# Kernel optimization log

Measured on AMD Instinct MI355X. Metric: run time of the kernel, lower is better.

## Reference

```python
import jax, jax.numpy as jnp
import numpy as np

N_U = 100000   # user nodes
N_V = 100000   # item nodes
D = 64         # input_dim
O = 64         # output_dim
R = 5          # num_support (rating levels)
E = 500000     # edges per relation


def setup_inputs() -> dict:
    key = jax.random.key(0)
    ks = jax.random.split(key, 8)
    init_range = np.sqrt(6.0 / (D + O))
    return {
        "x_u": jax.random.normal(ks[0], (N_U, D), jnp.float32),
        "x_v": jax.random.normal(ks[1], (N_V, D), jnp.float32),
        "weights_u": jax.random.uniform(ks[2], (R, D, O), jnp.float32, -init_range, init_range),
        "weights_v": jax.random.uniform(ks[3], (R, D, O), jnp.float32, -init_range, init_range),
        "bias_u": jnp.full((O,), 0.01, jnp.float32),
        "bias_v": jnp.full((O,), 0.01, jnp.float32),
        "edge_val": jax.random.uniform(ks[4], (R, E), jnp.float32),
        "edge_u": jax.random.randint(ks[5], (R, E), 0, N_U, jnp.int32),
        "edge_v": jax.random.randint(ks[6], (R, E), 0, N_V, jnp.int32),
    }


def reference(x_u, x_v, weights_u, weights_v, bias_u, bias_v, edge_val, edge_u, edge_v):
    # Cumulative (ordinal mixture) weights: wu_i = sum_{j<=i} W_u[j]
    Wu = jnp.cumsum(weights_u, axis=0)          # [R, D, O]
    Wv = jnp.cumsum(weights_v, axis=0)          # [R, D, O]

    tmp_u = jnp.einsum("nd,rdo->rno", x_u, Wu)  # [R, N_U, O]
    tmp_v = jnp.einsum("md,rdo->rmo", x_v, Wv)  # [R, N_V, O]

    gather = jax.vmap(lambda t, idx: t[idx])    # per-relation row gather

    # z_u = sum_r support_r @ tmp_v_r : scatter edge messages into user rows
    msg_u = (edge_val[..., None] * gather(tmp_v, edge_v)).reshape(R * E, O)
    z_u = jax.ops.segment_sum(msg_u, edge_u.reshape(-1), num_segments=N_U)

    # z_v = sum_r support_r^T @ tmp_u_r : scatter into item rows
    msg_v = (edge_val[..., None] * gather(tmp_u, edge_u)).reshape(R * E, O)
    z_v = jax.ops.segment_sum(msg_v, edge_v.reshape(-1), num_segments=N_V)

    u_out = jax.nn.relu(z_u + bias_u)
    v_out = jax.nn.relu(z_v + bias_v)
    return (u_out, v_out)
```

## Files before the change

kernel.cpp:

```cpp
#include <hip/hip_runtime.h>

#define N_U 100000
#define N_V 100000
#define OO 64
#define RR 5
#define EE 500000
#define TOT_E (RR * EE)
#define NB 782
#define CAP 4096
#define CAPU 3584
#define SCAT_BLOCKS 306
#define GEMM_BLOCKS 391

typedef short bf16x8 __attribute__((ext_vector_type(8)));
typedef float f32x4 __attribute__((ext_vector_type(4)));

__device__ __forceinline__ float bf2f(unsigned short u) {
  union { unsigned int i; float f; } x;
  x.i = ((unsigned int)u) << 16;
  return x.f;
}
__device__ __forceinline__ unsigned short f2bf(float f) {
  union { float f; unsigned int i; } x;
  x.f = f;
  unsigned int lsb = (x.i >> 16) & 1u;
  unsigned int r = x.i + 0x7fffu + lsb;
  return (unsigned short)(r >> 16);
}

__global__ void prep_weights(const float* __restrict__ wu,
                             const float* __restrict__ wv,
                             unsigned short* __restrict__ bfrag,
                             unsigned* __restrict__ gcur) {
  int side = blockIdx.x;
  if (gcur) {
    unsigned* g = gcur + side * 1024;
    for (int i = threadIdx.x; i < NB; i += 256) g[i] = (unsigned)i * CAP;
  }
  const float* w = side ? wv : wu;
  for (int idx = threadIdx.x; idx < 4096; idx += 256) {
    int d = idx >> 6, o = idx & 63;
    int c = o >> 4, n = o & 15;
    int sk = d >> 5, q = (d >> 3) & 3, jj = d & 7;
    int f = c * 2 + sk;
    int lane = q * 16 + n;
    int pos = (f * 64 + lane) * 8 + jj;
    float acc = 0.f;
    for (int r = 0; r < RR; ++r) {
      acc += w[r * 4096 + idx];
      bfrag[(side * RR + r) * 4096 + pos] = f2bf(acc);
    }
  }
}

__global__ __launch_bounds__(1024) void mega(
    const int* __restrict__ dst0, const int* __restrict__ src0,
    const int* __restrict__ dst1, const int* __restrict__ src1,
    const float* __restrict__ val,
    unsigned* __restrict__ gcur0, unsigned* __restrict__ keyP0,
    unsigned short* __restrict__ valP0,
    unsigned* __restrict__ gcur1, unsigned* __restrict__ keyP1,
    unsigned short* __restrict__ valP1,
    const float* __restrict__ X,
    const unsigned short* __restrict__ bfrag_side,
    unsigned short* __restrict__ tmp5,
    int nS0, int nS1) {
  __shared__ unsigned lds_u32[18972];
  int blk = blockIdx.x;
  int tid = threadIdx.x;
  if (blk < nS0 + nS1) {
    bool sB = (blk >= nS0);
    const int* dst = sB ? dst1 : dst0;
    const int* src = sB ? src1 : src0;
    unsigned* gcursor = sB ? gcur1 : gcur0;
    unsigned* keyP = sB ? keyP1 : keyP0;
    unsigned short* valP = sB ? valP1 : valP0;
    int sblk = sB ? blk - nS0 : blk;

    unsigned* skey = lds_u32;
    unsigned short* sval = (unsigned short*)(lds_u32 + 8192);
    unsigned short* sbid = (unsigned short*)(lds_u32 + 12288);
    unsigned* cnt  = lds_u32 + 16384;
    unsigned* sc   = lds_u32 + 17166;
    unsigned* gbase = lds_u32 + 18190;
    for (int i = tid; i < NB; i += 1024) cnt[i] = 0u;
    __syncthreads();
    int base = sblk * 8192;
    int t8 = base + tid * 8;
    bool full = (t8 < TOT_E);
    if (full) {
      int4 d0 = *(const int4*)(dst + t8);
      int4 d1 = *(const int4*)(dst + t8 + 4);
      atomicAdd(&cnt[d0.x >> 7], 1u);
      atomicAdd(&cnt[d0.y >> 7], 1u);
      atomicAdd(&cnt[d0.z >> 7], 1u);
      atomicAdd(&cnt[d0.w >> 7], 1u);
      atomicAdd(&cnt[d1.x >> 7], 1u);
      atomicAdd(&cnt[d1.y >> 7], 1u);
      atomicAdd(&cnt[d1.z >> 7], 1u);
      atomicAdd(&cnt[d1.w >> 7], 1u);
    }
    __syncthreads();
    sc[tid] = (tid < NB) ? cnt[tid] : 0u;
    __syncthreads();
    for (int off = 1; off < 1024; off <<= 1) {
      unsigned a = sc[tid];
      unsigned b = (tid >= off) ? sc[tid - off] : 0u;
      __syncthreads();
      sc[tid] = a + b;
      __syncthreads();
    }
    for (int b = tid; b < NB; b += 1024) {
      unsigned c = cnt[b];
      gbase[b] = c ? atomicAdd(&gcursor[b], c) : 0u;
      cnt[b] = sc[b] - c;
    }
    __syncthreads();
    unsigned total = sc[NB - 1];
    __syncthreads();
    for (int b = tid; b < NB; b += 1024) sc[b] = cnt[b];
    __syncthreads();
    if (full) {
      int4 d0 = *(const int4*)(dst + t8);
      int4 d1 = *(const int4*)(dst + t8 + 4);
      int4 s0 = *(const int4*)(src + t8);
      int4 s1 = *(const int4*)(src + t8 + 4);
      float4 v0 = *(const float4*)(val + t8);
      float4 v1 = *(const float4*)(val + t8 + 4);
      unsigned rb = (unsigned)(t8 / EE) * N_U;
#define PUT(dd, ss, vv)                                                     \
      {                                                                     \
        int bb = (dd) >> 7;                                                 \
        unsigned pos = atomicAdd(&sc[bb], 1u);                              \
        skey[pos] = (((unsigned)((dd) & 127)) << 19) | (rb + (unsigned)(ss)); \
        sval[pos] = f2bf(vv);                                               \
        sbid[pos] = (unsigned short)bb;                                     \
      }
      PUT(d0.x, s0.x, v0.x)
      PUT(d0.y, s0.y, v0.y)
      PUT(d0.z, s0.z, v0.z)
      PUT(d0.w, s0.w, v0.w)
      PUT(d1.x, s1.x, v1.x)
      PUT(d1.y, s1.y, v1.y)
      PUT(d1.z, s1.z, v1.z)
      PUT(d1.w, s1.w, v1.w)
#undef PUT
    }
    __syncthreads();
    for (int i = tid; i < (int)total; i += 1024) {
      unsigned b = sbid[i];
      unsigned addr = gbase[b] + ((unsigned)i - cnt[b]);
      keyP[addr] = skey[i];
      valP[addr] = sval[i];
    }
  } else {
    unsigned short* smem = (unsigned short*)lds_u32;
    for (int i = tid; i < 2560; i += 1024)
      ((bf16x8*)smem)[i] = ((const bf16x8*)bfrag_side)[i];
    __syncthreads();
    int lane = tid & 63;
    int wave = tid >> 6;
    int q = lane >> 4, m = lane & 15;
    int t = (blk - nS0 - nS1) * 16 + wave;
    if (t >= N_U / 16) return;
    int r0 = t * 16;
    const float* xr = X + (size_t)(r0 + m) * 64;
    float4 p0 = *(const float4*)(xr + q * 8);
    float4 p1 = *(const float4*)(xr + q * 8 + 4);
    float4 p2 = *(const float4*)(xr + 32 + q * 8);
    float4 p3 = *(const float4*)(xr + 32 + q * 8 + 4);
    bf16x8 a0, a1;
    a0[0] = (short)f2bf(p0.x); a0[1] = (short)f2bf(p0.y);
    a0[2] = (short)f2bf(p0.z); a0[3] = (short)f2bf(p0.w);
    a0[4] = (short)f2bf(p1.x); a0[5] = (short)f2bf(p1.y);
    a0[6] = (short)f2bf(p1.z); a0[7] = (short)f2bf(p1.w);
    a1[0] = (short)f2bf(p2.x); a1[1] = (short)f2bf(p2.y);
    a1[2] = (short)f2bf(p2.z); a1[3] = (short)f2bf(p2.w);
    a1[4] = (short)f2bf(p3.x); a1[5] = (short)f2bf(p3.y);
    a1[6] = (short)f2bf(p3.z); a1[7] = (short)f2bf(p3.w);
    for (int r = 0; r < RR; ++r) {
      f32x4 acc[4];
#pragma unroll
      for (int c = 0; c < 4; ++c) {
        bf16x8 b0 = *(const bf16x8*)(smem + r * 4096 + ((c * 2 + 0) * 64 + lane) * 8);
        bf16x8 b1 = *(const bf16x8*)(smem + r * 4096 + ((c * 2 + 1) * 64 + lane) * 8);
        f32x4 a = {0.f, 0.f, 0.f, 0.f};
        a = __builtin_amdgcn_mfma_f32_16x16x32_bf16(a0, b0, a, 0, 0, 0);
        a = __builtin_amdgcn_mfma_f32_16x16x32_bf16(a1, b1, a, 0, 0, 0);
        acc[c] = a;
      }
      unsigned short* trow = tmp5 + (size_t)r * N_U * 64;
#pragma unroll
      for (int i = 0; i < 4; ++i) {
        ushort4 o;
        o.x = f2bf(acc[0][i]); o.y = f2bf(acc[1][i]);
        o.z = f2bf(acc[2][i]); o.w = f2bf(acc[3][i]);
        *(ushort4*)(trow + (size_t)(r0 + q * 4 + i) * 64 + m * 4) = o;
      }
    }
  }
}

__global__ __launch_bounds__(512, 8) void bucket_sort_agg(
    const unsigned* __restrict__ keyP, const unsigned short* __restrict__ valP,
    const unsigned* __restrict__ gcursor,
    const unsigned short* __restrict__ tmp5,
    const float* __restrict__ bias, float* __restrict__ out) {
  __shared__ unsigned okey[CAP];
  __shared__ unsigned short oval[CAP];
  __shared__ unsigned hist[128];
  __shared__ unsigned starts[129];
  __shared__ unsigned cur[128];
  int b = blockIdx.x;
  unsigned base = (unsigned)b * CAP;
  int cnt = (int)(gcursor[b] - base);
  if (cnt > CAPU) cnt = CAPU;
  for (int i = threadIdx.x; i < 128; i += 512) hist[i] = 0u;
  __syncthreads();
  for (int i = threadIdx.x; i < cnt; i += 512)
    atomicAdd(&hist[keyP[base + i] >> 19], 1u);
  __syncthreads();
  if (threadIdx.x == 0) {
    unsigned acc = 0u;
    for (int l = 0; l < 128; ++l) {
      starts[l] = acc;
      acc += (hist[l] + 3u) & ~3u;
    }
    starts[128] = acc;
  }
  __syncthreads();
  unsigned tot = starts[128];
  for (int i = threadIdx.x; i < (int)tot; i += 512) { okey[i] = 0u; oval[i] = 0; }
  for (int l = threadIdx.x; l < 128; l += 512) cur[l] = starts[l];
  __syncthreads();
  for (int i = threadIdx.x; i < cnt; i += 512) {
    unsigned k = keyP[base + i];
    unsigned pos = atomicAdd(&cur[k >> 19], 1u);
    okey[pos] = k & 0x7FFFFu;
    oval[pos] = valP[base + i];
  }
  __syncthreads();

  int lane = threadIdx.x & 63;
  int wave = threadIdx.x >> 6;
  int g16 = lane >> 4;
  int m = lane & 15;
  int nb0 = b * 128;
  int nodes = (N_U - nb0 < 128) ? (N_U - nb0) : 128;
  const unsigned short* tp = tmp5 + (m << 2);
  float bl = bias[lane];
  for (int l = wave; l < nodes; l += 8) {
    unsigned s = starts[l];
    unsigned e = starts[l + 1];
    float a0 = 0.f, a1 = 0.f, a2 = 0.f, a3 = 0.f;
    unsigned k = s;
    for (; k + 8 <= e; k += 8) {
      unsigned key0 = okey[k + g16];
      unsigned key1 = okey[k + 4 + g16];
      float v0 = bf2f(oval[k + g16]);
      float v1 = bf2f(oval[k + 4 + g16]);
      ushort4 t0 = *(const ushort4*)(tp + (size_t)key0 * 64);
      ushort4 t1 = *(const ushort4*)(tp + (size_t)key1 * 64);
      a0 += v0 * bf2f(t0.x);
      a1 += v0 * bf2f(t0.y);
      a2 += v0 * bf2f(t0.z);
      a3 += v0 * bf2f(t0.w);
      a0 += v1 * bf2f(t1.x);
      a1 += v1 * bf2f(t1.y);
      a2 += v1 * bf2f(t1.z);
      a3 += v1 * bf2f(t1.w);
    }
    if (k < e) {
      unsigned key0 = okey[k + g16];
      float v0 = bf2f(oval[k + g16]);
      ushort4 t0 = *(const ushort4*)(tp + (size_t)key0 * 64);
      a0 += v0 * bf2f(t0.x);
      a1 += v0 * bf2f(t0.y);
      a2 += v0 * bf2f(t0.z);
      a3 += v0 * bf2f(t0.w);
    }
    a0 += __shfl_xor(a0, 16); a0 += __shfl_xor(a0, 32);
    a1 += __shfl_xor(a1, 16); a1 += __shfl_xor(a1, 32);
    a2 += __shfl_xor(a2, 16); a2 += __shfl_xor(a2, 32);
    a3 += __shfl_xor(a3, 16); a3 += __shfl_xor(a3, 32);
    float r = (g16 & 2) ? ((g16 & 1) ? a3 : a2) : ((g16 & 1) ? a1 : a0);
    out[(size_t)(nb0 + l) * 64 + lane] = fmaxf(r + bl, 0.f);
  }
}

__global__ __launch_bounds__(256) void gemm_kernel(
    const float* __restrict__ X, const unsigned short* __restrict__ bfrag,
    unsigned short* __restrict__ tmp) {
  int lane = threadIdx.x & 63;
  int wave = threadIdx.x >> 6;
  int q = lane >> 4, m = lane & 15;
  bf16x8 bf[8];
#pragma unroll
  for (int f = 0; f < 8; ++f)
    bf[f] = *(const bf16x8*)(bfrag + (f * 64 + lane) * 8);
  int t = blockIdx.x * 4 + wave;
  if (t >= N_U / 16) return;
  int r0 = t * 16;
  const float* xr = X + (size_t)(r0 + m) * 64;
  float4 p0 = *(const float4*)(xr + q * 8);
  float4 p1 = *(const float4*)(xr + q * 8 + 4);
  float4 p2 = *(const float4*)(xr + 32 + q * 8);
  float4 p3 = *(const float4*)(xr + 32 + q * 8 + 4);
  bf16x8 a0, a1;
  a0[0] = (short)f2bf(p0.x); a0[1] = (short)f2bf(p0.y);
  a0[2] = (short)f2bf(p0.z); a0[3] = (short)f2bf(p0.w);
  a0[4] = (short)f2bf(p1.x); a0[5] = (short)f2bf(p1.y);
  a0[6] = (short)f2bf(p1.z); a0[7] = (short)f2bf(p1.w);
  a1[0] = (short)f2bf(p2.x); a1[1] = (short)f2bf(p2.y);
  a1[2] = (short)f2bf(p2.z); a1[3] = (short)f2bf(p2.w);
  a1[4] = (short)f2bf(p3.x); a1[5] = (short)f2bf(p3.y);
  a1[6] = (short)f2bf(p3.z); a1[7] = (short)f2bf(p3.w);
#pragma unroll
  for (int c = 0; c < 4; ++c) {
    f32x4 acc = {0.f, 0.f, 0.f, 0.f};
    acc = __builtin_amdgcn_mfma_f32_16x16x32_bf16(a0, bf[c * 2 + 0], acc, 0, 0, 0);
    acc = __builtin_amdgcn_mfma_f32_16x16x32_bf16(a1, bf[c * 2 + 1], acc, 0, 0, 0);
#pragma unroll
    for (int i = 0; i < 4; ++i)
      tmp[(size_t)(r0 + q * 4 + i) * 64 + c * 16 + m] = f2bf(acc[i]);
  }
}

__global__ __launch_bounds__(256) void scatter_kernel(
    const unsigned short* __restrict__ tmp, const float* __restrict__ edge_val,
    const int* __restrict__ dst_idx, const int* __restrict__ src_idx,
    float* __restrict__ z, int base, int cnt) {
  int e = blockIdx.x * 4 + (threadIdx.x >> 6);
  int j = threadIdx.x & 63;
  int d = dst_idx[e] - base;
  if ((unsigned)d >= (unsigned)cnt) return;
  int s = src_idx[e];
  float w = edge_val[e];
  atomicAdd(&z[(size_t)d * 64 + j], w * bf2f(tmp[(size_t)s * 64 + j]));
}

__global__ __launch_bounds__(256) void finalize_kernel(
    const float* __restrict__ z, const float* __restrict__ bias,
    float* __restrict__ out) {
  size_t i4 = ((size_t)blockIdx.x * 256 + threadIdx.x) * 4;
  float4 zz = *(const float4*)(z + i4);
  const float4 bb = *(const float4*)(bias + (i4 & 63));
  float4 o;
  o.x = fmaxf(zz.x + bb.x, 0.f);
  o.y = fmaxf(zz.y + bb.y, 0.f);
  o.z = fmaxf(zz.z + bb.z, 0.f);
  o.w = fmaxf(zz.w + bb.w, 0.f);
  *(float4*)(out + i4) = o;
}

extern "C" void kernel_launch(void* const* d_in, const int* in_sizes, int n_in,
                              void* d_out, int out_size, void* d_ws, size_t ws_size,
                              hipStream_t stream) {
  const float* x_u      = (const float*)d_in[0];
  const float* x_v      = (const float*)d_in[1];
  const float* w_u      = (const float*)d_in[2];
  const float* w_v      = (const float*)d_in[3];
  const float* bias_u   = (const float*)d_in[4];
  const float* bias_v   = (const float*)d_in[5];
  const float* edge_val = (const float*)d_in[6];
  const int*   edge_u   = (const int*)d_in[7];
  const int*   edge_v   = (const int*)d_in[8];
  float* out = (float*)d_out;
  char* ws = (char*)d_ws;

  const size_t FAST_NEED = 83763200;

  unsigned short* bfrag = (unsigned short*)ws;

  if (ws_size >= FAST_NEED) {
    unsigned short* tmp5  = (unsigned short*)(ws + 131072);
    unsigned*       gcur  = (unsigned*)(ws + 64131072);
    unsigned*       keyP0 = (unsigned*)(ws + 64544768);
    unsigned short* valP0 = (unsigned short*)(ws + 77357056);
    unsigned*       keyP1 = (unsigned*)out;
    unsigned short* valP1 = (unsigned short*)((char*)out + 12812288);
    unsigned* gcur0 = gcur;
    unsigned* gcur1 = gcur + 1024;

    prep_weights<<<2, 256, 0, stream>>>(w_u, w_v, bfrag, gcur);

    mega<<<SCAT_BLOCKS * 2 + GEMM_BLOCKS, 1024, 0, stream>>>(
        edge_u, edge_v, edge_v, edge_u, edge_val,
        gcur0, keyP0, valP0, gcur1, keyP1, valP1,
        x_u, bfrag , tmp5, SCAT_BLOCKS, SCAT_BLOCKS);

    bucket_sort_agg<<<NB, 512, 0, stream>>>(keyP1, valP1, gcur1, tmp5,
                                            bias_v, out + (size_t)N_U * OO);

    mega<<<GEMM_BLOCKS, 1024, 0, stream>>>(
        edge_u, edge_v, edge_v, edge_u, edge_val,
        gcur0, keyP0, valP0, gcur1, keyP1, valP1,
        x_v, bfrag + RR * 4096 , tmp5, 0, 0);

    bucket_sort_agg<<<NB, 512, 0, stream>>>(keyP0, valP0, gcur0, tmp5,
                                            bias_u, out);
    return;
  }

  prep_weights<<<2, 256, 0, stream>>>(w_u, w_v, bfrag, (unsigned*)0);

  unsigned short* tmp = (unsigned short*)(ws + 131072);
  float*          z   = (float*)(ws + 131072 + 12800000);
  const size_t fixed = 131072 + 12800000;
  size_t zbytes = ws_size > fixed ? ws_size - fixed : 0;
  long chunk = (long)(zbytes / (OO * 4));
  chunk -= chunk % 16;
  if (chunk < 16) chunk = 16;
  if (chunk > N_U) chunk = N_U;

  const int gemm_grid = (N_U / 16 + 3) / 4;
  const int scat_grid = EE / 4;

  for (int side = 0; side < 2; ++side) {
    const float* X = side ? x_u : x_v;
    const unsigned short* frag0 = bfrag + (side ? 0 : RR * 4096);
    const int* dst = side ? edge_v : edge_u;
    const int* src = side ? edge_u : edge_v;
    const float* bias = side ? bias_v : bias_u;
    float* out_side = out + (size_t)side * N_U * OO;

    for (long base = 0; base < N_U; base += chunk) {
      long cnt = N_U - base < chunk ? N_U - base : chunk;
      hipMemsetAsync(z, 0, (size_t)cnt * OO * 4, stream);
      for (int r = 0; r < RR; ++r) {
        gemm_kernel<<<gemm_grid, 256, 0, stream>>>(X, frag0 + r * 4096, tmp);
        scatter_kernel<<<scat_grid, 256, 0, stream>>>(
            tmp, edge_val + (size_t)r * EE, dst + (size_t)r * EE,
            src + (size_t)r * EE, z, (int)base, (int)cnt);
      }
      finalize_kernel<<<(int)(cnt / 16), 256, 0, stream>>>(
          z, bias, out_side + base * OO);
    }
  }
}
```

Measured before the change: 316.3 us.

## Aggregate raw bf16 features per relation then apply weights via MFMA

Reorders the computation so that per-relation neighbour aggregation runs on bf16-converted raw input features, and the per-relation weight matmul is applied afterward inside the aggregation kernel via MFMA. This removes materialisation of the five-relation transformed tmp tensors (large write and gather traffic), so gathers read 64-wide bf16 rows from a single 12.8MB table instead of five. Both sides run in one fused agg_mm launch rather than alternating gemm and aggregation kernels. Costs: finer 640-bin per-relation sort, an extra bf16 rounding of the aggregated sums before the matmul, and per-wave MFMA work that depends on fixed 16-node tiles.

```diff
diff --git a/kernel.cpp b/kernel.cpp
--- a/kernel.cpp
+++ b/kernel.cpp
@@ -10,7 +10,8 @@
 #define CAP 4096
 #define CAPU 3584
 #define SCAT_BLOCKS 306
-#define GEMM_BLOCKS 391
+#define XCONV_BLOCKS 160
+#define BINS 640
 
 typedef short bf16x8 __attribute__((ext_vector_type(8)));
 typedef float f32x4 __attribute__((ext_vector_type(4)));
@@ -61,9 +62,8 @@
     unsigned short* __restrict__ valP0,
     unsigned* __restrict__ gcur1, unsigned* __restrict__ keyP1,
     unsigned short* __restrict__ valP1,
-    const float* __restrict__ X,
-    const unsigned short* __restrict__ bfrag_side,
-    unsigned short* __restrict__ tmp5,
+    const float* __restrict__ xu, const float* __restrict__ xv,
+    unsigned short* __restrict__ xbu, unsigned short* __restrict__ xbv,
     int nS0, int nS1) {
   __shared__ unsigned lds_u32[18972];
   int blk = blockIdx.x;
@@ -127,12 +127,12 @@
       int4 s1 = *(const int4*)(src + t8 + 4);
       float4 v0 = *(const float4*)(val + t8);
       float4 v1 = *(const float4*)(val + t8 + 4);
-      unsigned rb = (unsigned)(t8 / EE) * N_U;
+      unsigned rb = (unsigned)(t8 / EE) << 19;
 #define PUT(dd, ss, vv)                                                     \
       {                                                                     \
         int bb = (dd) >> 7;                                                 \
         unsigned pos = atomicAdd(&sc[bb], 1u);                              \
-        skey[pos] = (((unsigned)((dd) & 127)) << 19) | (rb + (unsigned)(ss)); \
+        skey[pos] = (((unsigned)((dd) & 127)) << 22) | rb | (unsigned)(ss); \
         sval[pos] = f2bf(vv);                                               \
         sbid[pos] = (unsigned short)bb;                                     \
       }
@@ -154,137 +154,130 @@
       valP[addr] = sval[i];
     }
   } else {
-    unsigned short* smem = (unsigned short*)lds_u32;
-    for (int i = tid; i < 2560; i += 1024)
-      ((bf16x8*)smem)[i] = ((const bf16x8*)bfrag_side)[i];
-    __syncthreads();
-    int lane = tid & 63;
-    int wave = tid >> 6;
-    int q = lane >> 4, m = lane & 15;
-    int t = (blk - nS0 - nS1) * 16 + wave;
-    if (t >= N_U / 16) return;
-    int r0 = t * 16;
-    const float* xr = X + (size_t)(r0 + m) * 64;
-    float4 p0 = *(const float4*)(xr + q * 8);
-    float4 p1 = *(const float4*)(xr + q * 8 + 4);
-    float4 p2 = *(const float4*)(xr + 32 + q * 8);
-    float4 p3 = *(const float4*)(xr + 32 + q * 8 + 4);
-    bf16x8 a0, a1;
-    a0[0] = (short)f2bf(p0.x); a0[1] = (short)f2bf(p0.y);
-    a0[2] = (short)f2bf(p0.z); a0[3] = (short)f2bf(p0.w);
-    a0[4] = (short)f2bf(p1.x); a0[5] = (short)f2bf(p1.y);
-    a0[6] = (short)f2bf(p1.z); a0[7] = (short)f2bf(p1.w);
-    a1[0] = (short)f2bf(p2.x); a1[1] = (short)f2bf(p2.y);
-    a1[2] = (short)f2bf(p2.z); a1[3] = (short)f2bf(p2.w);
-    a1[4] = (short)f2bf(p3.x); a1[5] = (short)f2bf(p3.y);
-    a1[6] = (short)f2bf(p3.z); a1[7] = (short)f2bf(p3.w);
-    for (int r = 0; r < RR; ++r) {
-      f32x4 acc[4];
-#pragma unroll
-      for (int c = 0; c < 4; ++c) {
-        bf16x8 b0 = *(const bf16x8*)(smem + r * 4096 + ((c * 2 + 0) * 64 + lane) * 8);
-        bf16x8 b1 = *(const bf16x8*)(smem + r * 4096 + ((c * 2 + 1) * 64 + lane) * 8);
-        f32x4 a = {0.f, 0.f, 0.f, 0.f};
-        a = __builtin_amdgcn_mfma_f32_16x16x32_bf16(a0, b0, a, 0, 0, 0);
-        a = __builtin_amdgcn_mfma_f32_16x16x32_bf16(a1, b1, a, 0, 0, 0);
-        acc[c] = a;
-      }
-      unsigned short* trow = tmp5 + (size_t)r * N_U * 64;
-#pragma unroll
-      for (int i = 0; i < 4; ++i) {
-        ushort4 o;
-        o.x = f2bf(acc[0][i]); o.y = f2bf(acc[1][i]);
-        o.z = f2bf(acc[2][i]); o.w = f2bf(acc[3][i]);
-        *(ushort4*)(trow + (size_t)(r0 + q * 4 + i) * 64 + m * 4) = o;
-      }
-    }
-  }
-}
-
-__global__ __launch_bounds__(512, 8) void bucket_sort_agg(
-    const unsigned* __restrict__ keyP, const unsigned short* __restrict__ valP,
-    const unsigned* __restrict__ gcursor,
-    const unsigned short* __restrict__ tmp5,
-    const float* __restrict__ bias, float* __restrict__ out) {
-  __shared__ unsigned okey[CAP];
-  __shared__ unsigned short oval[CAP];
-  __shared__ unsigned hist[128];
-  __shared__ unsigned starts[129];
-  __shared__ unsigned cur[128];
-  int b = blockIdx.x;
+    const int NF4 = (N_U * 64) / 4;
+    int xblk = blk - nS0 - nS1;
+    for (int i = xblk * 1024 + tid; i < 2 * NF4; i += XCONV_BLOCKS * 1024) {
+      bool sv = (i >= NF4);
+      int j = sv ? i - NF4 : i;
+      float4 f = ((const float4*)(sv ? xv : xu))[j];
+      ushort4 o;
+      o.x = f2bf(f.x); o.y = f2bf(f.y); o.z = f2bf(f.z); o.w = f2bf(f.w);
+      *(ushort4*)((sv ? xbv : xbu) + j * 4) = o;
+    }
+  }
+}
+
+__global__ __launch_bounds__(512, 6) void agg_mm(
+    const unsigned* __restrict__ keyP0, const unsigned short* __restrict__ valP0,
+    const unsigned* __restrict__ gcur0, const unsigned short* __restrict__ xb0,
+    const unsigned short* __restrict__ bfragA,
+    const float* __restrict__ bias0, float* __restrict__ out0,
+    const unsigned* __restrict__ keyP1, const unsigned short* __restrict__ valP1,
+    const unsigned* __restrict__ gcur1, const unsigned short* __restrict__ xb1,
+    const unsigned short* __restrict__ bfragB,
+    const float* __restrict__ bias1, float* __restrict__ out1) {
+  __shared__ unsigned okey[CAPU];
+  __shared__ unsigned short oval[CAPU];
+  __shared__ unsigned hist[BINS];
+  __shared__ unsigned starts[BINS + 1];
+  __shared__ unsigned cur[BINS];
+  __shared__ unsigned short A_lds[8][16][64];
+  int blk = blockIdx.x;
+  bool sB = (blk >= NB);
+  int b = sB ? blk - NB : blk;
+  const unsigned* keyP = sB ? keyP1 : keyP0;
+  const unsigned short* valP = sB ? valP1 : valP0;
+  const unsigned* gcursor = sB ? gcur1 : gcur0;
+  const unsigned short* xb = sB ? xb1 : xb0;
+  const unsigned short* bfragS = sB ? bfragB : bfragA;
+  const float* bias = sB ? bias1 : bias0;
+  float* out = sB ? out1 : out0;
+
   unsigned base = (unsigned)b * CAP;
   int cnt = (int)(gcursor[b] - base);
   if (cnt > CAPU) cnt = CAPU;
-  for (int i = threadIdx.x; i < 128; i += 512) hist[i] = 0u;
+  for (int i = threadIdx.x; i < BINS; i += 512) hist[i] = 0u;
   __syncthreads();
-  for (int i = threadIdx.x; i < cnt; i += 512)
-    atomicAdd(&hist[keyP[base + i] >> 19], 1u);
+  for (int i = threadIdx.x; i < cnt; i += 512) {
+    unsigned k = keyP[base + i];
+    unsigned bin = ((k >> 19) & 7u) * 128u + ((k >> 22) & 127u);
+    atomicAdd(&hist[bin], 1u);
+  }
   __syncthreads();
   if (threadIdx.x == 0) {
     unsigned acc = 0u;
-    for (int l = 0; l < 128; ++l) {
-      starts[l] = acc;
-      acc += (hist[l] + 3u) & ~3u;
-    }
-    starts[128] = acc;
+    for (int l = 0; l < BINS; ++l) { starts[l] = acc; acc += hist[l]; }
+    starts[BINS] = acc;
   }
   __syncthreads();
-  unsigned tot = starts[128];
-  for (int i = threadIdx.x; i < (int)tot; i += 512) { okey[i] = 0u; oval[i] = 0; }
-  for (int l = threadIdx.x; l < 128; l += 512) cur[l] = starts[l];
+  for (int l = threadIdx.x; l < BINS; l += 512) cur[l] = starts[l];
   __syncthreads();
   for (int i = threadIdx.x; i < cnt; i += 512) {
     unsigned k = keyP[base + i];
-    unsigned pos = atomicAdd(&cur[k >> 19], 1u);
-    okey[pos] = k & 0x7FFFFu;
+    unsigned bin = ((k >> 19) & 7u) * 128u + ((k >> 22) & 127u);
+    unsigned pos = atomicAdd(&cur[bin], 1u);
+    okey[pos] = k & 0x1FFFFu;
     oval[pos] = valP[base + i];
   }
   __syncthreads();
 
   int lane = threadIdx.x & 63;
-  int wave = threadIdx.x >> 6;
+  int wv = threadIdx.x >> 6;
   int g16 = lane >> 4;
   int m = lane & 15;
   int nb0 = b * 128;
-  int nodes = (N_U - nb0 < 128) ? (N_U - nb0) : 128;
-  const unsigned short* tp = tmp5 + (m << 2);
-  float bl = bias[lane];
-  for (int l = wave; l < nodes; l += 8) {
-    unsigned s = starts[l];
-    unsigned e = starts[l + 1];
-    float a0 = 0.f, a1 = 0.f, a2 = 0.f, a3 = 0.f;
-    unsigned k = s;
-    for (; k + 8 <= e; k += 8) {
-      unsigned key0 = okey[k + g16];
-      unsigned key1 = okey[k + 4 + g16];
-      float v0 = bf2f(oval[k + g16]);
-      float v1 = bf2f(oval[k + 4 + g16]);
-      ushort4 t0 = *(const ushort4*)(tp + (size_t)key0 * 64);
-      ushort4 t1 = *(const ushort4*)(tp + (size_t)key1 * 64);
-      a0 += v0 * bf2f(t0.x);
-      a1 += v0 * bf2f(t0.y);
-      a2 += v0 * bf2f(t0.z);
-      a3 += v0 * bf2f(t0.w);
-      a0 += v1 * bf2f(t1.x);
-      a1 += v1 * bf2f(t1.y);
-      a2 += v1 * bf2f(t1.z);
-      a3 += v1 * bf2f(t1.w);
-    }
-    if (k < e) {
-      unsigned key0 = okey[k + g16];
-      float v0 = bf2f(oval[k + g16]);
-      ushort4 t0 = *(const ushort4*)(tp + (size_t)key0 * 64);
-      a0 += v0 * bf2f(t0.x);
-      a1 += v0 * bf2f(t0.y);
-      a2 += v0 * bf2f(t0.z);
-      a3 += v0 * bf2f(t0.w);
-    }
-    a0 += __shfl_xor(a0, 16); a0 += __shfl_xor(a0, 32);
-    a1 += __shfl_xor(a1, 16); a1 += __shfl_xor(a1, 32);
-    a2 += __shfl_xor(a2, 16); a2 += __shfl_xor(a2, 32);
-    a3 += __shfl_xor(a3, 16); a3 += __shfl_xor(a3, 32);
-    float r = (g16 & 2) ? ((g16 & 1) ? a3 : a2) : ((g16 & 1) ? a1 : a0);
-    out[(size_t)(nb0 + l) * 64 + lane] = fmaxf(r + bl, 0.f);
+  const unsigned short* xp = xb + (m << 2);
+  f32x4 accO[4];
+#pragma unroll
+  for (int c = 0; c < 4; ++c) accO[c] = (f32x4){0.f, 0.f, 0.f, 0.f};
+
+  for (int r = 0; r < RR; ++r) {
+    for (int t = 0; t < 16; ++t) {
+      int l = wv * 16 + t;
+      unsigned s = starts[r * 128 + l];
+      unsigned e = starts[r * 128 + l + 1];
+      float a0 = 0.f, a1 = 0.f, a2 = 0.f, a3 = 0.f;
+      for (unsigned k = s; k < e; k += 4) {
+        unsigned idx = k + (unsigned)g16;
+        bool ok = idx < e;
+        unsigned j = ok ? idx : s;
+        unsigned srcn = okey[j];
+        float v = ok ? bf2f(oval[j]) : 0.f;
+        ushort4 t4 = *(const ushort4*)(xp + (size_t)srcn * 64);
+        a0 += v * bf2f(t4.x);
+        a1 += v * bf2f(t4.y);
+        a2 += v * bf2f(t4.z);
+        a3 += v * bf2f(t4.w);
+      }
+      a0 += __shfl_xor(a0, 16); a0 += __shfl_xor(a0, 32);
+      a1 += __shfl_xor(a1, 16); a1 += __shfl_xor(a1, 32);
+      a2 += __shfl_xor(a2, 16); a2 += __shfl_xor(a2, 32);
+      a3 += __shfl_xor(a3, 16); a3 += __shfl_xor(a3, 32);
+      if (g16 == 0) {
+        ushort4 o;
+        o.x = f2bf(a0); o.y = f2bf(a1); o.z = f2bf(a2); o.w = f2bf(a3);
+        *(ushort4*)&A_lds[wv][t][m << 2] = o;
+      }
+    }
+    bf16x8 af0 = *(const bf16x8*)&A_lds[wv][m][g16 * 8];
+    bf16x8 af1 = *(const bf16x8*)&A_lds[wv][m][32 + g16 * 8];
+#pragma unroll
+    for (int c = 0; c < 4; ++c) {
+      bf16x8 b0 = *(const bf16x8*)(bfragS + r * 4096 + ((c * 2 + 0) * 64 + lane) * 8);
+      bf16x8 b1 = *(const bf16x8*)(bfragS + r * 4096 + ((c * 2 + 1) * 64 + lane) * 8);
+      accO[c] = __builtin_amdgcn_mfma_f32_16x16x32_bf16(af0, b0, accO[c], 0, 0, 0);
+      accO[c] = __builtin_amdgcn_mfma_f32_16x16x32_bf16(af1, b1, accO[c], 0, 0, 0);
+    }
+  }
+#pragma unroll
+  for (int c = 0; c < 4; ++c) {
+    float bb = bias[c * 16 + m];
+#pragma unroll
+    for (int i = 0; i < 4; ++i) {
+      int node = nb0 + wv * 16 + g16 * 4 + i;
+      if (node < N_U)
+        out[(size_t)node * 64 + c * 16 + m] = fmaxf(accO[c][i] + bb, 0.f);
+    }
   }
 }
 
@@ -373,32 +366,27 @@
   unsigned short* bfrag = (unsigned short*)ws;
 
   if (ws_size >= FAST_NEED) {
-    unsigned short* tmp5  = (unsigned short*)(ws + 131072);
-    unsigned*       gcur  = (unsigned*)(ws + 64131072);
-    unsigned*       keyP0 = (unsigned*)(ws + 64544768);
-    unsigned short* valP0 = (unsigned short*)(ws + 77357056);
-    unsigned*       keyP1 = (unsigned*)out;
-    unsigned short* valP1 = (unsigned short*)((char*)out + 12812288);
+    unsigned short* xbu   = (unsigned short*)(ws + 131072);
+    unsigned short* xbv   = (unsigned short*)(ws + 12931072);
+    unsigned*       gcur  = (unsigned*)(ws + 25731072);
+    unsigned*       keyP0 = (unsigned*)(ws + 25739264);
+    unsigned short* valP0 = (unsigned short*)(ws + 38551552);
+    unsigned*       keyP1 = (unsigned*)(ws + 44957696);
+    unsigned short* valP1 = (unsigned short*)(ws + 57769984);
     unsigned* gcur0 = gcur;
     unsigned* gcur1 = gcur + 1024;
 
     prep_weights<<<2, 256, 0, stream>>>(w_u, w_v, bfrag, gcur);
 
-    mega<<<SCAT_BLOCKS * 2 + GEMM_BLOCKS, 1024, 0, stream>>>(
+    mega<<<SCAT_BLOCKS * 2 + XCONV_BLOCKS, 1024, 0, stream>>>(
         edge_u, edge_v, edge_v, edge_u, edge_val,
         gcur0, keyP0, valP0, gcur1, keyP1, valP1,
-        x_u, bfrag , tmp5, SCAT_BLOCKS, SCAT_BLOCKS);
-
-    bucket_sort_agg<<<NB, 512, 0, stream>>>(keyP1, valP1, gcur1, tmp5,
-                                            bias_v, out + (size_t)N_U * OO);
-
-    mega<<<GEMM_BLOCKS, 1024, 0, stream>>>(
-        edge_u, edge_v, edge_v, edge_u, edge_val,
-        gcur0, keyP0, valP0, gcur1, keyP1, valP1,
-        x_v, bfrag + RR * 4096 , tmp5, 0, 0);
-
-    bucket_sort_agg<<<NB, 512, 0, stream>>>(keyP0, valP0, gcur0, tmp5,
-                                            bias_u, out);
+        x_u, x_v, xbu, xbv, SCAT_BLOCKS, SCAT_BLOCKS);
+
+    agg_mm<<<NB * 2, 512, 0, stream>>>(
+        keyP0, valP0, gcur0, xbv, bfrag + RR * 4096, bias_u, out,
+        keyP1, valP1, gcur1, xbu, bfrag,             bias_v,
+        out + (size_t)N_U * OO);
     return;
   }
 
```

Result: slower. 435.2 us (+37.6%).
